# Kernel tuning notes

Hardware: AMD Instinct MI355X
Metric: run time of the kernel (lower is better)

## Reference

```python
import jax, jax.numpy as jnp
import numpy as np

PAD = -10000.0
B, N, F = 512, 2048, 16
H_PHI, LAT, H_RHO = 128, 128, 128


def _xavier(key, fan_in, fan_out):
    bound = np.sqrt(6.0 / (fan_in + fan_out))
    return jax.random.uniform(key, (fan_in, fan_out), jnp.float32, -bound, bound)


def setup_inputs() -> dict:
    key = jax.random.key(0)
    ks = jax.random.split(key, 12)
    x = jax.random.normal(ks[0], (B, N, F), jnp.float32)
    # ragged set lengths: pad tail rows with -10000.0 (the module's padding sentinel)
    lengths = jax.random.randint(ks[1], (B,), 1, N + 1)
    pad_mask = jnp.arange(N)[None, :] >= lengths[:, None]  # True where padded
    x = jnp.where(pad_mask[:, :, None], PAD, x)
    params = {
        "phi_w0": _xavier(ks[2], F, H_PHI), "phi_b0": jnp.zeros((H_PHI,), jnp.float32),
        "phi_w1": _xavier(ks[3], H_PHI, H_PHI), "phi_b1": jnp.zeros((H_PHI,), jnp.float32),
        "phi_w2": _xavier(ks[4], H_PHI, H_PHI), "phi_b2": jnp.zeros((H_PHI,), jnp.float32),
        "phi_w3": _xavier(ks[5], H_PHI, LAT), "phi_b3": jnp.zeros((LAT,), jnp.float32),
        "rho_w0": _xavier(ks[6], LAT, H_RHO), "rho_b0": jnp.zeros((H_RHO,), jnp.float32),
        "rho_w1": _xavier(ks[7], H_RHO, H_RHO), "rho_b1": jnp.zeros((H_RHO,), jnp.float32),
        "rho_w2": _xavier(ks[8], H_RHO, H_RHO), "rho_b2": jnp.zeros((H_RHO,), jnp.float32),
        "rho_w3": _xavier(ks[9], H_RHO, 1), "rho_b3": jnp.zeros((1,), jnp.float32),
    }
    return {"inputs": x, **params}


def reference(inputs, phi_w0, phi_b0, phi_w1, phi_b1, phi_w2, phi_b2, phi_w3, phi_b3,
              rho_w0, rho_b0, rho_w1, rho_b1, rho_w2, rho_b2, rho_w3, rho_b3):
    b, n, f = inputs.shape
    # valid-prefix mask: sum rows before the FIRST all-(-10000) row (matches torch loop)
    is_pad = jnp.all(inputs == PAD, axis=-1)                       # [B,N]
    first = jnp.where(jnp.any(is_pad, axis=-1), jnp.argmax(is_pad, axis=-1), n)
    mask = (jnp.arange(n)[None, :] < first[:, None]).astype(inputs.dtype)  # [B,N]
    relu = jax.nn.relu
    # phi applied per point
    h = relu(inputs @ phi_w0 + phi_b0)
    h = relu(h @ phi_w1 + phi_b1)
    h = relu(h @ phi_w2 + phi_b2)
    h = relu(h @ phi_w3 + phi_b3)                                  # [B,N,LAT]
    # masked variable-length sum pooling (segment reduce)
    pooled = jnp.einsum('bnd,bn->bd', h, mask)                     # [B,LAT]
    r = relu(pooled @ rho_w0 + rho_b0)
    r = relu(r @ rho_w1 + rho_b1)
    r = relu(r @ rho_w2 + rho_b2)
    cost = (r @ rho_w3 + rho_b3)[:, 0]                             # [B]
    return cost
```

## Files before the change

### kernel.cpp

```cpp
#include <hip/hip_runtime.h>

typedef _Float16 f16;
typedef f16  f16x2  __attribute__((ext_vector_type(2)));
typedef f16  f16x8  __attribute__((ext_vector_type(8)));
typedef __fp16 h16x2 __attribute__((ext_vector_type(2)));
typedef float f32x16 __attribute__((ext_vector_type(16)));

#define B_   512
#define N_   2048
#define PADV -10000.0f

union F16x8 { f16x8 v; f16x2 h2[4]; };

__device__ __forceinline__ f16x2 pkrtz(float a, float b) {
    h16x2 r = __builtin_amdgcn_cvt_pkrtz(a, b);
    return __builtin_bit_cast(f16x2, r);
}

__global__ void prep_kernel(const float* __restrict__ w0, const float* __restrict__ w1,
                            const float* __restrict__ w2, const float* __restrict__ w3,
                            f16* __restrict__ out, float* __restrict__ pooled)
{
    int i = blockIdx.x * 256 + threadIdx.x;
    if (i < 2048) {
        out[i] = (f16)w0[(i & 15) * 128 + (i >> 4)];
    } else if (i < 51200) {
        int j = i - 2048;
        int l = j >> 14, r = j & 16383;
        int o = r >> 7, slot = r & 127;
        int s = slot >> 4, qq = (slot >> 3) & 1, jj = slot & 7;
        int sig = 32 * (s >> 1) + 16 * (s & 1) + 4 * qq + 8 * (jj >> 2) + (jj & 3);
        const float* w = (l == 0) ? w1 : (l == 1) ? w2 : w3;
        out[i] = (f16)w[sig * 128 + o];
    }
    pooled[i] = 0.f;
}

__device__ __forceinline__ int swz(int row, int chunk) {
    return row * 256 + ((chunk ^ (row & 15)) << 4);
}

__device__ __forceinline__ void gl_lds16(const void* g, void* l) {
    __builtin_amdgcn_global_load_lds(
        (const __attribute__((address_space(1))) void*)g,
        (__attribute__((address_space(3))) void*)l, 16, 0, 0);
}

__global__ __launch_bounds__(256, 2) void phi_pool_kernel(
    const float* __restrict__ x,
    const f16*  __restrict__ wtbuf,
    const float* __restrict__ pb0, const float* __restrict__ pb1,
    const float* __restrict__ pb2, const float* __restrict__ pb3,
    float* __restrict__ pooled)
{
    __shared__ f16 wA[16384];
    __shared__ f16 wB[16384];

    const int tid  = threadIdx.x;
    const int lane = tid & 63;
    const int wv   = tid >> 6;
    const int l31  = lane & 31;
    const int q    = lane >> 5;
    const int b    = blockIdx.x & 511;
    const int tile0 = (blockIdx.x >> 9) * 256;

    {
        const float4 f0 = *(const float4*)(x + ((size_t)b * N_ + tile0) * 16);
        if (f0.x == PADV && f0.y == PADV && f0.z == PADV && f0.w == PADV) return;
    }

    const int p0 = tile0 + wv * 64;

    const float* xp = x + ((size_t)b * N_ + (size_t)(p0 + l31)) * 16 + 8 * q;
    float4 a0 = ((const float4*)xp)[0];
    float4 a1 = ((const float4*)xp)[1];
    float4 c0 = ((const float4*)(xp + 512))[0];
    float4 c1 = ((const float4*)(xp + 512))[1];

    f16x8 w0f[4];
    #pragma unroll
    for (int c = 0; c < 4; ++c)
        w0f[c] = *(const f16x8*)(wtbuf + (32 * c + l31) * 16 + 8 * q);

    {
        const f16* wl1 = wtbuf + 2048;
        const f16* wl2 = wtbuf + 2048 + 16384;
        #pragma unroll
        for (int i = 0; i < 8; ++i) {
            const int row   = wv * 32 + i * 4 + (lane >> 4);
            const int chunk = (lane & 15) ^ (row & 15);
            const int loff  = (wv * 32 + i * 4) * 256;
            gl_lds16(wl1 + row * 128 + chunk * 8, (char*)wA + loff);
            gl_lds16(wl2 + row * 128 + chunk * 8, (char*)wB + loff);
        }
    }

    bool vA = (a0.x != PADV) || (a0.y != PADV) || (a0.z != PADV) || (a0.w != PADV) ||
              (a1.x != PADV) || (a1.y != PADV) || (a1.z != PADV) || (a1.w != PADV);
    bool vB = (c0.x != PADV) || (c0.y != PADV) || (c0.z != PADV) || (c0.w != PADV) ||
              (c1.x != PADV) || (c1.y != PADV) || (c1.z != PADV) || (c1.w != PADV);
    unsigned long long blA = __ballot(vA), blB = __ballot(vB);
    const unsigned mA = (unsigned)blA | (unsigned)(blA >> 32);
    const unsigned mB = (unsigned)blB | (unsigned)(blB >> 32);

    F16x8 hf[2][8];
    hf[0][0].h2[0] = pkrtz(a0.x, a0.y);
    hf[0][0].h2[1] = pkrtz(a0.z, a0.w);
    hf[0][0].h2[2] = pkrtz(a1.x, a1.y);
    hf[0][0].h2[3] = pkrtz(a1.z, a1.w);
    hf[1][0].h2[0] = pkrtz(c0.x, c0.y);
    hf[1][0].h2[1] = pkrtz(c0.z, c0.w);
    hf[1][0].h2[2] = pkrtz(c1.x, c1.y);
    hf[1][0].h2[3] = pkrtz(c1.z, c1.w);

    f32x16 acc[2][4];

    #define INIT_ACC_BIAS(pb)                                              \
        {                                                                  \
            _Pragma("unroll")                                              \
            for (int c = 0; c < 4; ++c) {                                  \
                _Pragma("unroll")                                          \
                for (int g = 0; g < 4; ++g) {                              \
                    float4 bb = *(const float4*)((pb) + 32 * c + 8 * g + 4 * q); \
                    const float* bbp = (const float*)&bb;                  \
                    _Pragma("unroll")                                      \
                    for (int e = 0; e < 4; ++e) {                          \
                        acc[0][c][4 * g + e] = bbp[e];                     \
                        acc[1][c][4 * g + e] = bbp[e];                     \
                    }                                                      \
                }                                                          \
            }                                                              \
        }

    #define EPILOGUE()                                                     \
        {                                                                  \
            const f16x2 z2 = {(f16)0.f, (f16)0.f};                         \
            _Pragma("unroll")                                              \
            for (int t = 0; t < 2; ++t) {                                  \
                _Pragma("unroll")                                          \
                for (int s = 0; s < 8; ++s) {                              \
                    const int c = s >> 1, r0 = 8 * (s & 1);                \
                    _Pragma("unroll")                                      \
                    for (int p = 0; p < 4; ++p) {                          \
                        f16x2 m = pkrtz(                                   \
                            acc[t][c][r0 + 2 * p], acc[t][c][r0 + 2 * p + 1]); \
                        hf[t][s].h2[p] = __builtin_elementwise_max(m, z2); \
                    }                                                      \
                }                                                          \
            }                                                              \
        }

    INIT_ACC_BIAS(pb0);
    #pragma unroll
    for (int c = 0; c < 4; ++c) {
        acc[0][c] = __builtin_amdgcn_mfma_f32_32x32x16_f16(w0f[c], hf[0][0].v, acc[0][c], 0, 0, 0);
        acc[1][c] = __builtin_amdgcn_mfma_f32_32x32x16_f16(w0f[c], hf[1][0].v, acc[1][c], 0, 0, 0);
    }
    EPILOGUE();

    __syncthreads();

    INIT_ACC_BIAS(pb1);
    #pragma unroll
    for (int s = 0; s < 8; ++s) {
        f16x8 wf[4];
        #pragma unroll
        for (int c = 0; c < 4; ++c)
            wf[c] = *(const f16x8*)((const char*)wA + swz(32 * c + l31, 2 * s + q));
        #pragma unroll
        for (int c = 0; c < 4; ++c) {
            acc[0][c] = __builtin_amdgcn_mfma_f32_32x32x16_f16(wf[c], hf[0][s].v, acc[0][c], 0, 0, 0);
            acc[1][c] = __builtin_amdgcn_mfma_f32_32x32x16_f16(wf[c], hf[1][s].v, acc[1][c], 0, 0, 0);
        }
    }

    __syncthreads();

    {
        const f16* wl3 = wtbuf + 2048 + 32768;
        #pragma unroll
        for (int i = 0; i < 8; ++i) {
            const int row   = wv * 32 + i * 4 + (lane >> 4);
            const int chunk = (lane & 15) ^ (row & 15);
            const int loff  = (wv * 32 + i * 4) * 256;
            gl_lds16(wl3 + row * 128 + chunk * 8, (char*)wA + loff);
        }
    }

    EPILOGUE();

    INIT_ACC_BIAS(pb2);
    #pragma unroll
    for (int s = 0; s < 8; ++s) {
        f16x8 wf[4];
        #pragma unroll
        for (int c = 0; c < 4; ++c)
            wf[c] = *(const f16x8*)((const char*)wB + swz(32 * c + l31, 2 * s + q));
        #pragma unroll
        for (int c = 0; c < 4; ++c) {
            acc[0][c] = __builtin_amdgcn_mfma_f32_32x32x16_f16(wf[c], hf[0][s].v, acc[0][c], 0, 0, 0);
            acc[1][c] = __builtin_amdgcn_mfma_f32_32x32x16_f16(wf[c], hf[1][s].v, acc[1][c], 0, 0, 0);
        }
    }
    EPILOGUE();

    __syncthreads();

    {
        float bL[4];
        #pragma unroll
        for (int c = 0; c < 4; ++c) bL[c] = pb3[32 * c + l31];
        #pragma unroll
        for (int t = 0; t < 2; ++t)
            #pragma unroll
            for (int c = 0; c < 4; ++c)
                #pragma unroll
                for (int r = 0; r < 16; ++r) acc[t][c][r] = bL[c];
    }
    #pragma unroll
    for (int s = 0; s < 8; ++s) {
        f16x8 wf[4];
        #pragma unroll
        for (int c = 0; c < 4; ++c)
            wf[c] = *(const f16x8*)((const char*)wA + swz(32 * c + l31, 2 * s + q));
        #pragma unroll
        for (int c = 0; c < 4; ++c) {
            acc[0][c] = __builtin_amdgcn_mfma_f32_32x32x16_f16(hf[0][s].v, wf[c], acc[0][c], 0, 0, 0);
            acc[1][c] = __builtin_amdgcn_mfma_f32_32x32x16_f16(hf[1][s].v, wf[c], acc[1][c], 0, 0, 0);
        }
    }

    #pragma unroll
    for (int c = 0; c < 4; ++c) {
        float s0 = 0.f;
        #pragma unroll
        for (int t = 0; t < 2; ++t) {
            const unsigned m = t ? mB : mA;
            #pragma unroll
            for (int r = 0; r < 16; ++r) {
                const int ptl = 4 * q + (r & 3) + 8 * (r >> 2);
                float v = fmaxf(acc[t][c][r], 0.f);
                s0 += ((m >> ptl) & 1u) ? v : 0.f;
            }
        }
        s0 += __shfl_xor(s0, 32);
        if (q == 0) atomicAdd(&pooled[b * 128 + 32 * c + l31], s0);
    }
}

__global__ __launch_bounds__(128) void rho_kernel(
    const float* __restrict__ pooled,
    const float* __restrict__ w0, const float* __restrict__ b0,
    const float* __restrict__ w1, const float* __restrict__ b1,
    const float* __restrict__ w2, const float* __restrict__ b2,
    const float* __restrict__ w3, const float* __restrict__ b3,
    float* __restrict__ out)
{
    __shared__ float buf[2][128];
    __shared__ float red[2];
    const int b = blockIdx.x, t = threadIdx.x;
    buf[0][t] = pooled[b * 128 + t];
    __syncthreads();
    const float* ws3[3] = {w0, w1, w2};
    const float* bs3[3] = {b0, b1, b2};
    int cur = 0;
    #pragma unroll 1
    for (int l = 0; l < 3; ++l) {
        float acc = bs3[l][t];
        const float* w = ws3[l];
        #pragma unroll 8
        for (int k = 0; k < 128; ++k)
            acc = fmaf(buf[cur][k], w[k * 128 + t], acc);
        buf[cur ^ 1][t] = fmaxf(acc, 0.f);
        cur ^= 1;
        __syncthreads();
    }
    float v = buf[cur][t] * w3[t];
    #pragma unroll
    for (int off = 32; off > 0; off >>= 1)
        v += __shfl_down(v, off, 64);
    if ((t & 63) == 0) red[t >> 6] = v;
    __syncthreads();
    if (t == 0) out[b] = red[0] + red[1] + b3[0];
}

extern "C" void kernel_launch(void* const* d_in, const int* in_sizes, int n_in,
                              void* d_out, int out_size, void* d_ws, size_t ws_size,
                              hipStream_t stream)
{
    (void)in_sizes; (void)n_in; (void)out_size; (void)ws_size;
    const float* x      = (const float*)d_in[0];
    const float* phi_w0 = (const float*)d_in[1];
    const float* phi_b0 = (const float*)d_in[2];
    const float* phi_w1 = (const float*)d_in[3];
    const float* phi_b1 = (const float*)d_in[4];
    const float* phi_w2 = (const float*)d_in[5];
    const float* phi_b2 = (const float*)d_in[6];
    const float* phi_w3 = (const float*)d_in[7];
    const float* phi_b3 = (const float*)d_in[8];
    const float* rho_w0 = (const float*)d_in[9];
    const float* rho_b0 = (const float*)d_in[10];
    const float* rho_w1 = (const float*)d_in[11];
    const float* rho_b1 = (const float*)d_in[12];
    const float* rho_w2 = (const float*)d_in[13];
    const float* rho_b2 = (const float*)d_in[14];
    const float* rho_w3 = (const float*)d_in[15];
    const float* rho_b3 = (const float*)d_in[16];

    float* pooled = (float*)d_ws;
    f16*   wtbuf  = (f16*)((char*)d_ws + 262144);

    prep_kernel<<<256, 256, 0, stream>>>(phi_w0, phi_w1, phi_w2, phi_w3, wtbuf, pooled);
    phi_pool_kernel<<<4096, 256, 0, stream>>>(x, wtbuf, phi_b0, phi_b1, phi_b2, phi_b3, pooled);
    rho_kernel<<<B_, 128, 0, stream>>>(pooled, rho_w0, rho_b0, rho_w1, rho_b1,
                                       rho_w2, rho_b2, rho_w3, rho_b3, (float*)d_out);
}
```

Measured before the change: 204.5 us.

## Halve per-wave tile, read layers 2-3 weights from global in fragment layout

Each wave now processes 32 points instead of 64, halving accumulator and activation registers, and the grid doubles to 8192 blocks. Only layer-1 weights stay in LDS (32KB instead of 64KB); layers 2 and 3 are pre-swizzled by the prep kernel into per-lane MFMA fragment order and loaded directly from global/L2. Launch bounds raise to 3 blocks/CU, and waves with no valid points exit early after layer 0. The trade is more redundant global weight traffic and more blocks in exchange for higher occupancy and fewer barriers.

```diff
diff --git a/kernel.cpp b/kernel.cpp
--- a/kernel.cpp
+++ b/kernel.cpp
@@ -24,14 +24,24 @@
     int i = blockIdx.x * 256 + threadIdx.x;
     if (i < 2048) {
         out[i] = (f16)w0[(i & 15) * 128 + (i >> 4)];
-    } else if (i < 51200) {
-        int j = i - 2048;
-        int l = j >> 14, r = j & 16383;
+    } else if (i < 18432) {
+        int r = i - 2048;
         int o = r >> 7, slot = r & 127;
         int s = slot >> 4, qq = (slot >> 3) & 1, jj = slot & 7;
         int sig = 32 * (s >> 1) + 16 * (s & 1) + 4 * qq + 8 * (jj >> 2) + (jj & 3);
-        const float* w = (l == 0) ? w1 : (l == 1) ? w2 : w3;
-        out[i] = (f16)w[sig * 128 + o];
+        out[i] = (f16)w1[sig * 128 + o];
+    } else if (i < 51200) {
+        int k = i - 18432;
+        const float* w = (k < 16384) ? w2 : w3;
+        k &= 16383;
+        int jj   = k & 7;
+        int lane = (k >> 3) & 63;
+        int sc   = k >> 9;
+        int s = sc >> 2, c = sc & 3;
+        int row = 32 * c + (lane & 31);
+        int qq  = lane >> 5;
+        int sig = 32 * (s >> 1) + 16 * (s & 1) + 4 * qq + 8 * (jj >> 2) + (jj & 3);
+        out[i] = (f16)w[sig * 128 + row];
     }
     pooled[i] = 0.f;
 }
@@ -46,7 +56,7 @@
         (__attribute__((address_space(3))) void*)l, 16, 0, 0);
 }
 
-__global__ __launch_bounds__(256, 2) void phi_pool_kernel(
+__global__ __launch_bounds__(256, 3) void phi_pool_kernel(
     const float* __restrict__ x,
     const f16*  __restrict__ wtbuf,
     const float* __restrict__ pb0, const float* __restrict__ pb1,
@@ -54,7 +64,6 @@
     float* __restrict__ pooled)
 {
     __shared__ f16 wA[16384];
-    __shared__ f16 wB[16384];
 
     const int tid  = threadIdx.x;
     const int lane = tid & 63;
@@ -62,20 +71,16 @@
     const int l31  = lane & 31;
     const int q    = lane >> 5;
     const int b    = blockIdx.x & 511;
-    const int tile0 = (blockIdx.x >> 9) * 256;
+    const int tile0 = (blockIdx.x >> 9) * 128;
 
     {
         const float4 f0 = *(const float4*)(x + ((size_t)b * N_ + tile0) * 16);
         if (f0.x == PADV && f0.y == PADV && f0.z == PADV && f0.w == PADV) return;
     }
 
-    const int p0 = tile0 + wv * 64;
-
-    const float* xp = x + ((size_t)b * N_ + (size_t)(p0 + l31)) * 16 + 8 * q;
+    const float* xp = x + ((size_t)b * N_ + (size_t)(tile0 + wv * 32 + l31)) * 16 + 8 * q;
     float4 a0 = ((const float4*)xp)[0];
     float4 a1 = ((const float4*)xp)[1];
-    float4 c0 = ((const float4*)(xp + 512))[0];
-    float4 c1 = ((const float4*)(xp + 512))[1];
 
     f16x8 w0f[4];
     #pragma unroll
@@ -84,36 +89,27 @@
 
     {
         const f16* wl1 = wtbuf + 2048;
-        const f16* wl2 = wtbuf + 2048 + 16384;
         #pragma unroll
         for (int i = 0; i < 8; ++i) {
             const int row   = wv * 32 + i * 4 + (lane >> 4);
             const int chunk = (lane & 15) ^ (row & 15);
             const int loff  = (wv * 32 + i * 4) * 256;
             gl_lds16(wl1 + row * 128 + chunk * 8, (char*)wA + loff);
-            gl_lds16(wl2 + row * 128 + chunk * 8, (char*)wB + loff);
         }
     }
 
     bool vA = (a0.x != PADV) || (a0.y != PADV) || (a0.z != PADV) || (a0.w != PADV) ||
               (a1.x != PADV) || (a1.y != PADV) || (a1.z != PADV) || (a1.w != PADV);
-    bool vB = (c0.x != PADV) || (c0.y != PADV) || (c0.z != PADV) || (c0.w != PADV) ||
-              (c1.x != PADV) || (c1.y != PADV) || (c1.z != PADV) || (c1.w != PADV);
-    unsigned long long blA = __ballot(vA), blB = __ballot(vB);
+    unsigned long long blA = __ballot(vA);
     const unsigned mA = (unsigned)blA | (unsigned)(blA >> 32);
-    const unsigned mB = (unsigned)blB | (unsigned)(blB >> 32);
-
-    F16x8 hf[2][8];
-    hf[0][0].h2[0] = pkrtz(a0.x, a0.y);
-    hf[0][0].h2[1] = pkrtz(a0.z, a0.w);
-    hf[0][0].h2[2] = pkrtz(a1.x, a1.y);
-    hf[0][0].h2[3] = pkrtz(a1.z, a1.w);
-    hf[1][0].h2[0] = pkrtz(c0.x, c0.y);
-    hf[1][0].h2[1] = pkrtz(c0.z, c0.w);
-    hf[1][0].h2[2] = pkrtz(c1.x, c1.y);
-    hf[1][0].h2[3] = pkrtz(c1.z, c1.w);
-
-    f32x16 acc[2][4];
+
+    F16x8 hf[8];
+    hf[0].h2[0] = pkrtz(a0.x, a0.y);
+    hf[0].h2[1] = pkrtz(a0.z, a0.w);
+    hf[0].h2[2] = pkrtz(a1.x, a1.y);
+    hf[0].h2[3] = pkrtz(a1.z, a1.w);
+
+    f32x16 acc[4];
 
     #define INIT_ACC_BIAS(pb)                                              \
         {                                                                  \
@@ -124,10 +120,8 @@
                     float4 bb = *(const float4*)((pb) + 32 * c + 8 * g + 4 * q); \
                     const float* bbp = (const float*)&bb;                  \
                     _Pragma("unroll")                                      \
-                    for (int e = 0; e < 4; ++e) {                          \
-                        acc[0][c][4 * g + e] = bbp[e];                     \
-                        acc[1][c][4 * g + e] = bbp[e];                     \
-                    }                                                      \
+                    for (int e = 0; e < 4; ++e)                            \
+                        acc[c][4 * g + e] = bbp[e];                        \
                 }                                                          \
             }                                                              \
         }
@@ -136,29 +130,25 @@
         {                                                                  \
             const f16x2 z2 = {(f16)0.f, (f16)0.f};                         \
             _Pragma("unroll")                                              \
-            for (int t = 0; t < 2; ++t) {                                  \
+            for (int s = 0; s < 8; ++s) {                                  \
+                const int c = s >> 1, r0 = 8 * (s & 1);                    \
                 _Pragma("unroll")                                          \
-                for (int s = 0; s < 8; ++s) {                              \
-                    const int c = s >> 1, r0 = 8 * (s & 1);                \
-                    _Pragma("unroll")                                      \
-                    for (int p = 0; p < 4; ++p) {                          \
-                        f16x2 m = pkrtz(                                   \
-                            acc[t][c][r0 + 2 * p], acc[t][c][r0 + 2 * p + 1]); \
-                        hf[t][s].h2[p] = __builtin_elementwise_max(m, z2); \
-                    }                                                      \
+                for (int p = 0; p < 4; ++p) {                              \
+                    f16x2 m = pkrtz(acc[c][r0 + 2 * p], acc[c][r0 + 2 * p + 1]); \
+                    hf[s].h2[p] = __builtin_elementwise_max(m, z2);        \
                 }                                                          \
             }                                                              \
         }
 
     INIT_ACC_BIAS(pb0);
     #pragma unroll
-    for (int c = 0; c < 4; ++c) {
-        acc[0][c] = __builtin_amdgcn_mfma_f32_32x32x16_f16(w0f[c], hf[0][0].v, acc[0][c], 0, 0, 0);
-        acc[1][c] = __builtin_amdgcn_mfma_f32_32x32x16_f16(w0f[c], hf[1][0].v, acc[1][c], 0, 0, 0);
-    }
+    for (int c = 0; c < 4; ++c)
+        acc[c] = __builtin_amdgcn_mfma_f32_32x32x16_f16(w0f[c], hf[0].v, acc[c], 0, 0, 0);
     EPILOGUE();
 
     __syncthreads();
+
+    if (mA == 0u) return;
 
     INIT_ACC_BIAS(pb1);
     #pragma unroll
@@ -168,80 +158,54 @@
         for (int c = 0; c < 4; ++c)
             wf[c] = *(const f16x8*)((const char*)wA + swz(32 * c + l31, 2 * s + q));
         #pragma unroll
-        for (int c = 0; c < 4; ++c) {
-            acc[0][c] = __builtin_amdgcn_mfma_f32_32x32x16_f16(wf[c], hf[0][s].v, acc[0][c], 0, 0, 0);
-            acc[1][c] = __builtin_amdgcn_mfma_f32_32x32x16_f16(wf[c], hf[1][s].v, acc[1][c], 0, 0, 0);
-        }
-    }
-
-    __syncthreads();
-
-    {
-        const f16* wl3 = wtbuf + 2048 + 32768;
-        #pragma unroll
-        for (int i = 0; i < 8; ++i) {
-            const int row   = wv * 32 + i * 4 + (lane >> 4);
-            const int chunk = (lane & 15) ^ (row & 15);
-            const int loff  = (wv * 32 + i * 4) * 256;
-            gl_lds16(wl3 + row * 128 + chunk * 8, (char*)wA + loff);
-        }
-    }
-
+        for (int c = 0; c < 4; ++c)
+            acc[c] = __builtin_amdgcn_mfma_f32_32x32x16_f16(wf[c], hf[s].v, acc[c], 0, 0, 0);
+    }
     EPILOGUE();
 
+    const f16* w2x = wtbuf + 18432;
     INIT_ACC_BIAS(pb2);
     #pragma unroll
     for (int s = 0; s < 8; ++s) {
         f16x8 wf[4];
         #pragma unroll
         for (int c = 0; c < 4; ++c)
-            wf[c] = *(const f16x8*)((const char*)wB + swz(32 * c + l31, 2 * s + q));
-        #pragma unroll
-        for (int c = 0; c < 4; ++c) {
-            acc[0][c] = __builtin_amdgcn_mfma_f32_32x32x16_f16(wf[c], hf[0][s].v, acc[0][c], 0, 0, 0);
-            acc[1][c] = __builtin_amdgcn_mfma_f32_32x32x16_f16(wf[c], hf[1][s].v, acc[1][c], 0, 0, 0);
-        }
+            wf[c] = *(const f16x8*)(w2x + ((s * 4 + c) * 64 + lane) * 8);
+        #pragma unroll
+        for (int c = 0; c < 4; ++c)
+            acc[c] = __builtin_amdgcn_mfma_f32_32x32x16_f16(wf[c], hf[s].v, acc[c], 0, 0, 0);
     }
     EPILOGUE();
 
-    __syncthreads();
-
+    const f16* w3x = wtbuf + 34816;
     {
         float bL[4];
         #pragma unroll
         for (int c = 0; c < 4; ++c) bL[c] = pb3[32 * c + l31];
         #pragma unroll
-        for (int t = 0; t < 2; ++t)
+        for (int c = 0; c < 4; ++c)
             #pragma unroll
-            for (int c = 0; c < 4; ++c)
-                #pragma unroll
-                for (int r = 0; r < 16; ++r) acc[t][c][r] = bL[c];
+            for (int r = 0; r < 16; ++r) acc[c][r] = bL[c];
     }
     #pragma unroll
     for (int s = 0; s < 8; ++s) {
         f16x8 wf[4];
         #pragma unroll
         for (int c = 0; c < 4; ++c)
-            wf[c] = *(const f16x8*)((const char*)wA + swz(32 * c + l31, 2 * s + q));
-        #pragma unroll
-        for (int c = 0; c < 4; ++c) {
-            acc[0][c] = __builtin_amdgcn_mfma_f32_32x32x16_f16(hf[0][s].v, wf[c], acc[0][c], 0, 0, 0);
-            acc[1][c] = __builtin_amdgcn_mfma_f32_32x32x16_f16(hf[1][s].v, wf[c], acc[1][c], 0, 0, 0);
-        }
+            wf[c] = *(const f16x8*)(w3x + ((s * 4 + c) * 64 + lane) * 8);
+        #pragma unroll
+        for (int c = 0; c < 4; ++c)
+            acc[c] = __builtin_amdgcn_mfma_f32_32x32x16_f16(hf[s].v, wf[c], acc[c], 0, 0, 0);
     }
 
     #pragma unroll
     for (int c = 0; c < 4; ++c) {
         float s0 = 0.f;
         #pragma unroll
-        for (int t = 0; t < 2; ++t) {
-            const unsigned m = t ? mB : mA;
-            #pragma unroll
-            for (int r = 0; r < 16; ++r) {
-                const int ptl = 4 * q + (r & 3) + 8 * (r >> 2);
-                float v = fmaxf(acc[t][c][r], 0.f);
-                s0 += ((m >> ptl) & 1u) ? v : 0.f;
-            }
+        for (int r = 0; r < 16; ++r) {
+            const int ptl = 4 * q + (r & 3) + 8 * (r >> 2);
+            float v = fmaxf(acc[c][r], 0.f);
+            s0 += ((mA >> ptl) & 1u) ? v : 0.f;
         }
         s0 += __shfl_xor(s0, 32);
         if (q == 0) atomicAdd(&pooled[b * 128 + 32 * c + l31], s0);
@@ -311,7 +275,7 @@
     f16*   wtbuf  = (f16*)((char*)d_ws + 262144);
 
     prep_kernel<<<256, 256, 0, stream>>>(phi_w0, phi_w1, phi_w2, phi_w3, wtbuf, pooled);
-    phi_pool_kernel<<<4096, 256, 0, stream>>>(x, wtbuf, phi_b0, phi_b1, phi_b2, phi_b3, pooled);
+    phi_pool_kernel<<<8192, 256, 0, stream>>>(x, wtbuf, phi_b0, phi_b1, phi_b2, phi_b3, pooled);
     rho_kernel<<<B_, 128, 0, stream>>>(pooled, rho_w0, rho_b0, rho_w1, rho_b1,
                                        rho_w2, rho_b2, rho_w3, rho_b3, (float*)d_out);
 }
```

After: 229.9 us. +12.4%, slower.

## Read layer-3 weights from global in lane-packed layout, drop LDS reload and barriers

Applied to the files above, without the earlier changes.

The prep kernel now packs the last phi layer's weights into a per-lane fragment order, so each wave can load its MFMA operands for that layer directly from global memory with coalesced 16-byte reads. This removes the LDS reload of layer-3 weights and two block-wide barriers in the middle of the kernel. Separately, a wave whose points are all padding now exits after the first shared barrier instead of running the remaining layers. The trade-off is more global/L2 traffic for layer 3, and an early exit placed after the last remaining barrier.

```diff
diff --git a/kernel.cpp b/kernel.cpp
--- a/kernel.cpp
+++ b/kernel.cpp
@@ -24,14 +24,24 @@
     int i = blockIdx.x * 256 + threadIdx.x;
     if (i < 2048) {
         out[i] = (f16)w0[(i & 15) * 128 + (i >> 4)];
-    } else if (i < 51200) {
-        int j = i - 2048;
-        int l = j >> 14, r = j & 16383;
+    } else if (i < 34816) {
+        int r = i - 2048;
+        const float* w = (r < 16384) ? w1 : w2;
+        r &= 16383;
         int o = r >> 7, slot = r & 127;
         int s = slot >> 4, qq = (slot >> 3) & 1, jj = slot & 7;
         int sig = 32 * (s >> 1) + 16 * (s & 1) + 4 * qq + 8 * (jj >> 2) + (jj & 3);
-        const float* w = (l == 0) ? w1 : (l == 1) ? w2 : w3;
         out[i] = (f16)w[sig * 128 + o];
+    } else if (i < 51200) {
+        int k = i - 34816;
+        int jj   = k & 7;
+        int lane = (k >> 3) & 63;
+        int sc   = k >> 9;
+        int s = sc >> 2, c = sc & 3;
+        int row = 32 * c + (lane & 31);
+        int qq  = lane >> 5;
+        int sig = 32 * (s >> 1) + 16 * (s & 1) + 4 * qq + 8 * (jj >> 2) + (jj & 3);
+        out[i] = (f16)w3[sig * 128 + row];
     }
     pooled[i] = 0.f;
 }
@@ -84,7 +94,7 @@
 
     {
         const f16* wl1 = wtbuf + 2048;
-        const f16* wl2 = wtbuf + 2048 + 16384;
+        const f16* wl2 = wtbuf + 18432;
         #pragma unroll
         for (int i = 0; i < 8; ++i) {
             const int row   = wv * 32 + i * 4 + (lane >> 4);
@@ -160,6 +170,8 @@
 
     __syncthreads();
 
+    if ((mA | mB) == 0u) return;
+
     INIT_ACC_BIAS(pb1);
     #pragma unroll
     for (int s = 0; s < 8; ++s) {
@@ -173,20 +185,6 @@
             acc[1][c] = __builtin_amdgcn_mfma_f32_32x32x16_f16(wf[c], hf[1][s].v, acc[1][c], 0, 0, 0);
         }
     }
-
-    __syncthreads();
-
-    {
-        const f16* wl3 = wtbuf + 2048 + 32768;
-        #pragma unroll
-        for (int i = 0; i < 8; ++i) {
-            const int row   = wv * 32 + i * 4 + (lane >> 4);
-            const int chunk = (lane & 15) ^ (row & 15);
-            const int loff  = (wv * 32 + i * 4) * 256;
-            gl_lds16(wl3 + row * 128 + chunk * 8, (char*)wA + loff);
-        }
-    }
-
     EPILOGUE();
 
     INIT_ACC_BIAS(pb2);
@@ -204,8 +202,7 @@
     }
     EPILOGUE();
 
-    __syncthreads();
-
+    const f16* w3x = wtbuf + 34816;
     {
         float bL[4];
         #pragma unroll
@@ -222,7 +219,7 @@
         f16x8 wf[4];
         #pragma unroll
         for (int c = 0; c < 4; ++c)
-            wf[c] = *(const f16x8*)((const char*)wA + swz(32 * c + l31, 2 * s + q));
+            wf[c] = *(const f16x8*)(w3x + ((s * 4 + c) * 64 + lane) * 8);
         #pragma unroll
         for (int c = 0; c < 4; ++c) {
             acc[0][c] = __builtin_amdgcn_mfma_f32_32x32x16_f16(hf[0][s].v, wf[c], acc[0][c], 0, 0, 0);
```

Result: no change. 205.8 us (+0.6%).
